# Kernel optimization log

Measured on AMD Instinct MI355X. Metric: run time of the kernel, lower is better.

## Reference

```python
import jax, jax.numpy as jnp
import numpy as np

# Model dims (hardcoded by the hw-accurate numerics: >>6 mean -> d_model=64, 45/256 ~ 1/sqrt(32) -> head_dim=32)
D_MODEL = 64; N_HEADS = 2; HEAD_DIM = 32; D_FF = 256
N_LAYERS = 4; VOCAB = 8192; CTX = 1024; B = 4; T = 1024


def _ste(x, y):
    # forward value y, straight-through gradient of x
    return x + jax.lax.stop_gradient(y - x)


def ste_round_clamp(x, lo, hi):
    return _ste(x, jnp.clip(jnp.round(x), lo, hi))


def ste_round_clamp_int8(x):
    return ste_round_clamp(x, -128.0, 127.0)


def ste_shift_right(x, n):
    s = x * (0.5 ** n)
    return _ste(s, jnp.floor(s))


def ste_hw_int8(x):
    # hardware truncation to signed 8 bits (wrap-around, not clamp)
    return _ste(x, jnp.mod(x + 128.0, 256.0) - 128.0)


def bitlinear_hw(x, w):
    # ternary weights via STE (BitNet b1.58 style), int accumulate, >>6 requant, int8 clamp
    scale = jnp.maximum(jnp.mean(jnp.abs(w)), 1e-5)
    w_t = ste_round_clamp(w / scale, -1.0, 1.0)
    acc = jnp.einsum('btc,oc->bto', x, w_t)
    return ste_round_clamp_int8(ste_shift_right(acc, 6))


def rmsnorm_hw(x, weight):
    x_int = ste_round_clamp_int8(x)
    sum_sq = jnp.sum(x_int * x_int, axis=-1, keepdims=True)
    mean_sq = ste_shift_right(sum_sq, 6)                       # /64 == /d_model
    lut_idx = jnp.clip(ste_shift_right(mean_sq, 6), 0.0, 255.0)
    bin_center = jnp.maximum(lut_idx * 64.0 + 32.0, 1.0)
    inv_rms = ste_round_clamp(16384.0 / jnp.sqrt(bin_center), 0.0, 16383.0)
    w_c = weight + jax.lax.stop_gradient(jnp.clip(weight, -2.0, 2.0) - weight)
    gamma_q = ste_round_clamp(w_c * 1024.0, -32768.0, 32767.0)  # Q5.10
    p1 = ste_shift_right(x_int * inv_rms, 8)
    y = ste_shift_right(p1 * gamma_q, 10)
    return ste_round_clamp_int8(y)


def hw_softmax(scores):
    # 4-segment piecewise-linear exp + uint8 normalization (Softmax.scala)
    m = jnp.max(scores, axis=-1, keepdims=True)
    sh = scores - m
    ea = jnp.where(sh >= -3.0, 256.0 + sh * 64.0,
         jnp.where(sh >= -8.0, 64.0 + (sh + 3.0) * 11.0,
         jnp.where(sh >= -24.0, sh + 24.0, 0.0)))
    s = jnp.maximum(jnp.sum(ea, axis=-1, keepdims=True), 1.0)
    return ste_round_clamp(ea / s * 255.0, 0.0, 255.0)


def _forward(tokens, tok_emb, pos_emb, attn_norm_w, q_w, k_w, v_w, o_w,
             ff_norm_w, up_w, down_w, final_norm_w):
    positions = jnp.arange(T)
    tok_q = ste_round_clamp(tok_emb[tokens] * 1024.0, -32768.0, 32767.0)
    pos_q = ste_round_clamp(pos_emb[positions] * 1024.0, -32768.0, 32767.0)
    x = ste_hw_int8(ste_shift_right(tok_q + pos_q[None], 3))   # [B,T,D]
    causal = jnp.triu(jnp.ones((T, T), dtype=bool), k=1)
    for i in range(N_LAYERS):
        # attention block
        h = rmsnorm_hw(x, attn_norm_w[i])
        q = bitlinear_hw(h, q_w[i]).reshape(B, T, N_HEADS, HEAD_DIM).transpose(0, 2, 1, 3)
        k = bitlinear_hw(h, k_w[i]).reshape(B, T, N_HEADS, HEAD_DIM).transpose(0, 2, 1, 3)
        v = bitlinear_hw(h, v_w[i]).reshape(B, T, N_HEADS, HEAD_DIM).transpose(0, 2, 1, 3)
        scores = ste_shift_right(jnp.einsum('bhqd,bhkd->bhqk', q, k) * 45.0, 8)
        scores = jnp.where(causal, -32767.0, scores)
        probs = hw_softmax(scores)                              # uint8-valued
        a = ste_hw_int8(ste_shift_right(jnp.einsum('bhqk,bhkd->bhqd', probs, v), 8))
        a = a.transpose(0, 2, 1, 3).reshape(B, T, D_MODEL)
        a = bitlinear_hw(a, o_w[i])
        x = ste_hw_int8(x + a)
        # FFN block
        h = rmsnorm_hw(x, ff_norm_w[i])
        u = ste_round_clamp_int8(jax.nn.relu(bitlinear_hw(h, up_w[i])))
        x = ste_hw_int8(x + bitlinear_hw(u, down_w[i]))
    x = rmsnorm_hw(x, final_norm_w)
    # hw logits: INT8 activations x Q5.10 tied embedding, dequant + 1/sqrt(d) scale
    emb_q = ste_round_clamp(tok_emb * 1024.0, -32768.0, 32767.0)
    logits = jnp.einsum('btd,vd->btv', x, emb_q) * (D_MODEL ** -0.5 / 1024.0)
    return logits


def setup_inputs() -> dict:
    key = jax.random.key(0)
    ks = jax.random.split(key, 12)
    std = 0.02
    inp = {
        'tokens': jax.random.randint(ks[0], (B, T), 0, VOCAB),
        'tok_emb': jax.random.normal(ks[1], (VOCAB, D_MODEL), jnp.float32),  # default N(0,1)
        'pos_emb': std * jax.random.normal(ks[2], (CTX, D_MODEL), jnp.float32),
        'attn_norm_w': jnp.ones((N_LAYERS, D_MODEL), jnp.float32),
        'q_w': std * jax.random.normal(ks[3], (N_LAYERS, D_MODEL, D_MODEL), jnp.float32),
        'k_w': std * jax.random.normal(ks[4], (N_LAYERS, D_MODEL, D_MODEL), jnp.float32),
        'v_w': std * jax.random.normal(ks[5], (N_LAYERS, D_MODEL, D_MODEL), jnp.float32),
        'o_w': std * jax.random.normal(ks[6], (N_LAYERS, D_MODEL, D_MODEL), jnp.float32),
        'ff_norm_w': jnp.ones((N_LAYERS, D_MODEL), jnp.float32),
        'up_w': std * jax.random.normal(ks[7], (N_LAYERS, D_FF, D_MODEL), jnp.float32),
        'down_w': std * jax.random.normal(ks[8], (N_LAYERS, D_MODEL, D_FF), jnp.float32),
        'final_norm_w': jnp.ones((D_MODEL,), jnp.float32),
    }
    return inp


def reference(tokens, tok_emb, pos_emb, attn_norm_w, q_w, k_w, v_w, o_w,
              ff_norm_w, up_w, down_w, final_norm_w):
    return _forward(tokens, tok_emb, pos_emb, attn_norm_w, q_w, k_w, v_w, o_w,
                    ff_norm_w, up_w, down_w, final_norm_w)
```

## Files before the change

kernel.cpp:

```cpp
#include <hip/hip_runtime.h>
#include <stdint.h>

#define T_CTX 1024
#define DM 64
#define NH 2
#define HD 32
#define DFF 256
#define NVOCAB 8192

typedef int v4i __attribute__((ext_vector_type(4)));

__device__ __forceinline__ int clampi(int v, int lo, int hi){ return v<lo?lo:(v>hi?hi:v); }
__device__ __forceinline__ int wrap8(int v){ return ((v + 128) & 255) - 128; }
__device__ __forceinline__ int sdot4(int a, int b, int c){ return __builtin_amdgcn_sdot4(a, b, c, false); }

__device__ __forceinline__ int wave_reduce_add(int v){
  #pragma unroll
  for (int off = 1; off < 64; off <<= 1) v += __shfl_xor(v, off, 64);
  return v;
}
__device__ __forceinline__ int wave_reduce_max(int v){
  #pragma unroll
  for (int off = 1; off < 64; off <<= 1){ int o = __shfl_xor(v, off, 64); v = o > v ? o : v; }
  return v;
}

__device__ __forceinline__ int rmsnorm_one(int xv, int g){
  int ss  = wave_reduce_add(xv * xv);
  int ms  = ss >> 6;
  int lut = ms >> 6; if (lut > 255) lut = 255;
  int bc  = lut * 64 + 32;
  int inv = (int)__builtin_rint(16384.0 / __builtin_sqrt((double)bc));
  int p1  = (xv * inv) >> 8;
  int y   = (p1 * g) >> 10;
  return clampi(y, -128, 127);
}

__global__ __launch_bounds__(256) void prep_embed(
    const int* __restrict__ tokens, const float* __restrict__ tok_emb, const float* __restrict__ pos_emb,
    const float* __restrict__ qw, const float* __restrict__ kw, const float* __restrict__ vw,
    const float* __restrict__ ow, const float* __restrict__ uw, const float* __restrict__ dw,
    const float* __restrict__ anw, const float* __restrict__ fnw, const float* __restrict__ finw,
    int8_t* __restrict__ wt, int16_t* __restrict__ gq,
    int8_t* __restrict__ elo, int8_t* __restrict__ ehi,
    int8_t* __restrict__ x, int8_t* __restrict__ qA, int8_t* __restrict__ kA, int8_t* __restrict__ vT)
{
  __shared__ double sred[256];
  __shared__ int8_t sh_h[4][64];
  int tid = threadIdx.x, bid = blockIdx.x;
  if (bid < 24) {
    int layer = bid / 6, kind = bid % 6;
    const float* src; int n; int off;
    switch (kind) {
      case 0:  src = qw + layer*4096;  n = 4096;  off = 0;     break;
      case 1:  src = kw + layer*4096;  n = 4096;  off = 4096;  break;
      case 2:  src = vw + layer*4096;  n = 4096;  off = 8192;  break;
      case 3:  src = ow + layer*4096;  n = 4096;  off = 12288; break;
      case 4:  src = uw + layer*16384; n = 16384; off = 16384; break;
      default: src = dw + layer*16384; n = 16384; off = 32768; break;
    }
    double s = 0.0;
    for (int i = tid; i < n; i += 256) s += (double)__builtin_fabsf(src[i]);
    sred[tid] = s; __syncthreads();
    for (int st = 128; st > 0; st >>= 1){ if (tid < st) sred[tid] += sred[tid + st]; __syncthreads(); }
    float fs = (float)(sred[0] / (double)n);
    if (fs < 1e-5f) fs = 1e-5f;
    int8_t* dst = wt + layer*49152 + off;
    for (int i = tid; i < n; i += 256) {
      int t = (int)__builtin_rintf(src[i] / fs);
      dst[i] = (int8_t)clampi(t, -1, 1);
    }
  } else if (bid == 24) {
    for (int i = tid; i < 576; i += 256) {
      int norm = i >> 6, c = i & 63;
      const float* wsrc = (norm < 4) ? (anw + norm*64) : (norm < 8) ? (fnw + (norm-4)*64) : finw;
      float wv = wsrc[c];
      float wc = wv < -2.0f ? -2.0f : (wv > 2.0f ? 2.0f : wv);
      gq[i] = (int16_t)clampi((int)__builtin_rintf(wc * 1024.0f), -32768, 32767);
    }
  } else if (bid < 2073) {
    int i = (bid - 25)*256 + tid;
    if (i < NVOCAB * DM) {
      int e  = clampi((int)__builtin_rintf(tok_emb[i] * 1024.0f), -32768, 32767);
      int l  = ((e + 128) & 255) - 128;
      int hh = (e - l) >> 8;
      if (hh > 127) hh = 127;
      elo[i] = (int8_t)l; ehi[i] = (int8_t)hh;
    }
  } else {
    int blk = bid - 2073;
    int w = tid >> 6, lane = tid & 63;
    float fss[3];
    const float* srcs[3] = { qw, kw, vw };
    for (int mtx = 0; mtx < 3; mtx++) {
      const float* src = srcs[mtx];
      double s = 0.0;
      for (int i = tid; i < 4096; i += 256) s += (double)__builtin_fabsf(src[i]);
      sred[tid] = s; __syncthreads();
      for (int st = 128; st > 0; st >>= 1){ if (tid < st) sred[tid] += sred[tid + st]; __syncthreads(); }
      float fs = (float)(sred[0] / 4096.0);
      if (fs < 1e-5f) fs = 1e-5f;
      fss[mtx] = fs;
      __syncthreads();
    }
    int wqr[16], wkr[16], wvr[16];
    {
      const float4* rq = (const float4*)(qw + lane*64);
      const float4* rk = (const float4*)(kw + lane*64);
      const float4* rv = (const float4*)(vw + lane*64);
      #pragma unroll
      for (int i = 0; i < 16; i++) {
        float4 f = rq[i];
        int t0 = clampi((int)__builtin_rintf(f.x / fss[0]), -1, 1);
        int t1 = clampi((int)__builtin_rintf(f.y / fss[0]), -1, 1);
        int t2 = clampi((int)__builtin_rintf(f.z / fss[0]), -1, 1);
        int t3 = clampi((int)__builtin_rintf(f.w / fss[0]), -1, 1);
        wqr[i] = (t0&255) | ((t1&255)<<8) | ((t2&255)<<16) | ((t3&255)<<24);
      }
      #pragma unroll
      for (int i = 0; i < 16; i++) {
        float4 f = rk[i];
        int t0 = clampi((int)__builtin_rintf(f.x / fss[1]), -1, 1);
        int t1 = clampi((int)__builtin_rintf(f.y / fss[1]), -1, 1);
        int t2 = clampi((int)__builtin_rintf(f.z / fss[1]), -1, 1);
        int t3 = clampi((int)__builtin_rintf(f.w / fss[1]), -1, 1);
        wkr[i] = (t0&255) | ((t1&255)<<8) | ((t2&255)<<16) | ((t3&255)<<24);
      }
      #pragma unroll
      for (int i = 0; i < 16; i++) {
        float4 f = rv[i];
        int t0 = clampi((int)__builtin_rintf(f.x / fss[2]), -1, 1);
        int t1 = clampi((int)__builtin_rintf(f.y / fss[2]), -1, 1);
        int t2 = clampi((int)__builtin_rintf(f.z / fss[2]), -1, 1);
        int t3 = clampi((int)__builtin_rintf(f.w / fss[2]), -1, 1);
        wvr[i] = (t0&255) | ((t1&255)<<8) | ((t2&255)<<16) | ((t3&255)<<24);
      }
    }
    float gw = anw[lane];
    float gc = gw < -2.0f ? -2.0f : (gw > 2.0f ? 2.0f : gw);
    int g = clampi((int)__builtin_rintf(gc * 1024.0f), -32768, 32767);
    #pragma unroll
    for (int pass = 0; pass < 2; pass++) {
      int t = blk*8 + pass*4 + w;
      int tok = tokens[t];
      int s = t & (T_CTX - 1);
      int tq = clampi((int)__builtin_rintf(tok_emb[tok*DM + lane] * 1024.0f), -32768, 32767);
      int pq = clampi((int)__builtin_rintf(pos_emb[s*DM + lane] * 1024.0f), -32768, 32767);
      int xv = wrap8((tq + pq) >> 3);
      x[t*DM + lane] = (int8_t)xv;
      int h = rmsnorm_one(xv, g);
      sh_h[w][lane] = (int8_t)h;
      const int* h4 = (const int*)sh_h[w];
      int b = t >> 10;
      int hh = lane >> 5, d = lane & 31;
      int bhh = b*NH + hh;
      {
        int acc = 0;
        #pragma unroll
        for (int i = 0; i < 16; i++) acc = sdot4(h4[i], wqr[i], acc);
        qA[(bhh*T_CTX + s)*HD + d] = (int8_t)clampi(acc >> 6, -128, 127);
      }
      {
        int acc = 0;
        #pragma unroll
        for (int i = 0; i < 16; i++) acc = sdot4(h4[i], wkr[i], acc);
        kA[(bhh*T_CTX + s)*HD + d] = (int8_t)clampi(acc >> 6, -128, 127);
      }
      {
        int acc = 0;
        #pragma unroll
        for (int i = 0; i < 16; i++) acc = sdot4(h4[i], wvr[i], acc);
        vT[(bhh*HD + d)*T_CTX + s] = (int8_t)clampi(acc >> 6, -128, 127);
      }
    }
  }
}

__global__ __launch_bounds__(512, 4) void layer_kernel(
    const int8_t* __restrict__ qA, const int8_t* __restrict__ kA, const int8_t* __restrict__ vT,
    int8_t* __restrict__ x, int8_t* __restrict__ qN, int8_t* __restrict__ kN, int8_t* __restrict__ vN,
    const int8_t* __restrict__ wt, const int16_t* __restrict__ gq, int8_t* __restrict__ xf,
    int L, int pre_layer, int do_final)
{
  __shared__ int vt32[64*256];
  __shared__ int sp32[8][256];
  __shared__ int sh_a32[4][16];
  __shared__ int8_t sh8[4][256];

  int tid = threadIdx.x;
  int w = tid >> 6, lane = tid & 63;
  int blk = blockIdx.x;
  int b = blk & 3;
  int s0 = 1020 - 4*(blk >> 2);
  int tl = w >> 1, h = w & 1;
  int qi = s0 + tl;
  int bh = b*NH + h;
  const int8_t* qBase = qA + bh*(T_CTX*HD);
  const int8_t* kBase = kA + bh*(T_CTX*HD);

  #pragma unroll
  for (int r = 0; r < 8; r++) {
    int rr = w*8 + r;
    int slot = rr >> 5, d = rr & 31;
    const int* src = (const int*)(vT + (b*NH + slot)*(HD*T_CTX) + d*T_CTX);
    int xw = ((d >> 2) & 3) << 3;
    int li = lane ^ xw;
    int* dstrow = vt32 + rr*256;
    int v0 = src[lane], v1 = src[lane+64], v2 = src[lane+128], v3 = src[lane+192];
    dstrow[li] = v0; dstrow[li+64] = v1; dstrow[li+128] = v2; dstrow[li+192] = v3;
  }

  const int4* qr = (const int4*)(qBase + qi*HD);
  int4 qa = qr[0], qb = qr[1];
  int sc[16];
  int mloc = -(1 << 30);
  #pragma unroll
  for (int j = 0; j < 16; j++) {
    int k = lane + j*64;
    int s;
    if (k <= qi) {
      const int4* kr = (const int4*)(kBase + k*HD);
      int4 ka = kr[0], kb = kr[1];
      int d = 0;
      d = sdot4(qa.x, ka.x, d); d = sdot4(qa.y, ka.y, d);
      d = sdot4(qa.z, ka.z, d); d = sdot4(qa.w, ka.w, d);
      d = sdot4(qb.x, kb.x, d); d = sdot4(qb.y, kb.y, d);
      d = sdot4(qb.z, kb.z, d); d = sdot4(qb.w, kb.w, d);
      s = (d * 45) >> 8;
    } else s = -(1 << 30);
    sc[j] = s; if (s > mloc) mloc = s;
  }
  int m = wave_reduce_max(mloc);
  int ssum = 0;
  #pragma unroll
  for (int j = 0; j < 16; j++) {
    int k = lane + j*64;
    int e = 0;
    if (k <= qi) {
      int sh = sc[j] - m;
      e = (sh >= -3) ? (256 + sh*64)
        : (sh >= -8) ? (64 + (sh + 3)*11)
        : (sh >= -24) ? (sh + 24) : 0;
    }
    sc[j] = e; ssum += e;
  }
  int s0sum = wave_reduce_add(ssum); if (s0sum < 1) s0sum = 1;
  float sf = (float)s0sum;
  uint8_t* spb = (uint8_t*)sp32[w];
  #pragma unroll
  for (int j = 0; j < 16; j++) {
    int k = lane + j*64;
    int p = (int)__builtin_rintf((float)sc[j] / sf * 255.0f);
    spb[k] = (uint8_t)clampi(p, 0, 255);
  }
  __syncthreads();

  int dg = lane & 7, kc = lane >> 3;
  int xw = (dg & 3) << 3;
  const int* vr0 = vt32 + (h*32 + dg*4 + 0)*256;
  const int* vr1 = vt32 + (h*32 + dg*4 + 1)*256;
  const int* vr2 = vt32 + (h*32 + dg*4 + 2)*256;
  const int* vr3 = vt32 + (h*32 + dg*4 + 3)*256;
  const int* spw = sp32[w];
  int hi0=0, hi1=0, hi2=0, hi3=0, lo0=0, lo1=0, lo2=0, lo3=0;
  int cmax = qi >> 2;
  for (int c = kc; c <= cmax; c += 8) {
    int p4 = spw[c];
    int cs = c ^ xw;
    int ph = (p4 >> 1) & 0x7f7f7f7f;
    int pl = p4 & 0x01010101;
    int v0 = vr0[cs], v1 = vr1[cs], v2 = vr2[cs], v3 = vr3[cs];
    hi0 = sdot4(ph, v0, hi0); lo0 = sdot4(pl, v0, lo0);
    hi1 = sdot4(ph, v1, hi1); lo1 = sdot4(pl, v1, lo1);
    hi2 = sdot4(ph, v2, hi2); lo2 = sdot4(pl, v2, lo2);
    hi3 = sdot4(ph, v3, hi3); lo3 = sdot4(pl, v3, lo3);
  }
  int a0 = 2*hi0 + lo0, a1 = 2*hi1 + lo1, a2 = 2*hi2 + lo2, a3 = 2*hi3 + lo3;
  #pragma unroll
  for (int off = 8; off < 64; off <<= 1) {
    a0 += __shfl_xor(a0, off, 64);
    a1 += __shfl_xor(a1, off, 64);
    a2 += __shfl_xor(a2, off, 64);
    a3 += __shfl_xor(a3, off, 64);
  }
  if (kc == 0) {
    int r0 = wrap8(a0 >> 8) & 255;
    int r1 = wrap8(a1 >> 8) & 255;
    int r2 = wrap8(a2 >> 8) & 255;
    int r3 = wrap8(a3 >> 8) & 255;
    int packed = r0 | (r1 << 8) | (r2 << 16) | (r3 << 24);
    sh_a32[tl][h*8 + dg] = packed;
  }
  __syncthreads();

  if (w < 4) {
    int t = b*T_CTX + s0 + w;
    const int8_t* wtL = wt + L*49152;
    int xv = (int)x[t*DM + lane];
    {
      const int* a4 = sh_a32[w];
      const int* wo = (const int*)(wtL + 12288);
      int acc = 0;
      #pragma unroll
      for (int i = 0; i < 16; i++) acc = sdot4(a4[i], wo[lane*16 + i], acc);
      xv = wrap8(xv + clampi(acc >> 6, -128, 127));
    }
    int h2 = rmsnorm_one(xv, (int)gq[(4 + L)*DM + lane]);
    int8_t* myS = sh8[w];
    myS[lane] = (int8_t)h2;
    const int* h4 = (const int*)myS;
    int uv[4];
    {
      const int* wu = (const int*)(wtL + 16384);
      #pragma unroll
      for (int jj = 0; jj < 4; jj++) {
        int j = jj*64 + lane;
        int acc = 0;
        #pragma unroll
        for (int i = 0; i < 16; i++) acc = sdot4(h4[i], wu[j*16 + i], acc);
        int u = clampi(acc >> 6, -128, 127);
        uv[jj] = u < 0 ? 0 : u;
      }
    }
    #pragma unroll
    for (int jj = 0; jj < 4; jj++) myS[jj*64 + lane] = (int8_t)uv[jj];
    {
      const int* u4 = (const int*)myS;
      const int* wd = (const int*)(wtL + 32768);
      int acc = 0;
      #pragma unroll
      for (int i = 0; i < 64; i++) acc = sdot4(u4[i], wd[lane*64 + i], acc);
      xv = wrap8(xv + clampi(acc >> 6, -128, 127));
    }
    x[t*DM + lane] = (int8_t)xv;
    if (pre_layer >= 0) {
      int hp = rmsnorm_one(xv, (int)gq[pre_layer*DM + lane]);
      myS[lane] = (int8_t)hp;
      const int* hp4 = (const int*)myS;
      const int8_t* wtP = wt + pre_layer*49152;
      int s = s0 + w;
      int hh = lane >> 5, d = lane & 31;
      int bhh = b*NH + hh;
      {
        const int* wm = (const int*)(wtP + 0);
        int acc = 0;
        #pragma unroll
        for (int i = 0; i < 16; i++) acc = sdot4(hp4[i], wm[lane*16 + i], acc);
        qN[(bhh*T_CTX + s)*HD + d] = (int8_t)clampi(acc >> 6, -128, 127);
      }
      {
        const int* wm = (const int*)(wtP + 4096);
        int acc = 0;
        #pragma unroll
        for (int i = 0; i < 16; i++) acc = sdot4(hp4[i], wm[lane*16 + i], acc);
        kN[(bhh*T_CTX + s)*HD + d] = (int8_t)clampi(acc >> 6, -128, 127);
      }
      {
        const int* wm = (const int*)(wtP + 8192);
        int acc = 0;
        #pragma unroll
        for (int i = 0; i < 16; i++) acc = sdot4(hp4[i], wm[lane*16 + i], acc);
        vN[(bhh*HD + d)*T_CTX + s] = (int8_t)clampi(acc >> 6, -128, 127);
      }
    }
    if (do_final) {
      int hf = rmsnorm_one(xv, (int)gq[8*DM + lane]);
      xf[t*DM + lane] = (int8_t)hf;
    }
  }
}

__global__ __launch_bounds__(256) void logits_kernel(
    const int8_t* __restrict__ xf, const int8_t* __restrict__ elo, const int8_t* __restrict__ ehi,
    float* __restrict__ out)
{
  int w = threadIdx.x >> 6, lane = threadIdx.x & 63;
  int m = lane & 15, quad = lane >> 4;
  int tokBase = blockIdx.y * 64 + w * 16;
  v4i Bx = *(const v4i*)(xf + (tokBase + m)*DM + quad*16);
  float* orow = out + (tokBase + m)*NVOCAB;
  #pragma unroll
  for (int tile = 0; tile < 8; tile++) {
    int vocBase = blockIdx.x * 128 + tile * 16;
    v4i Alo = *(const v4i*)(elo + (vocBase + m)*DM + quad*16);
    v4i Ahi = *(const v4i*)(ehi + (vocBase + m)*DM + quad*16);
    v4i zero = {0, 0, 0, 0};
    v4i dLo = __builtin_amdgcn_mfma_i32_16x16x64_i8(Alo, Bx, zero, 0, 0, 0);
    v4i dHi = __builtin_amdgcn_mfma_i32_16x16x64_i8(Ahi, Bx, zero, 0, 0, 0);
    float4 o;
    o.x = (float)(dLo[0] + (dHi[0] << 8)) * 1.220703125e-4f;
    o.y = (float)(dLo[1] + (dHi[1] << 8)) * 1.220703125e-4f;
    o.z = (float)(dLo[2] + (dHi[2] << 8)) * 1.220703125e-4f;
    o.w = (float)(dLo[3] + (dHi[3] << 8)) * 1.220703125e-4f;
    *(float4*)(orow + vocBase + quad*4) = o;
  }
}

extern "C" void kernel_launch(void* const* d_in, const int* in_sizes, int n_in,
                              void* d_out, int out_size, void* d_ws, size_t ws_size,
                              hipStream_t stream)
{
  const int*   tokens  = (const int*)d_in[0];
  const float* tok_emb = (const float*)d_in[1];
  const float* pos_emb = (const float*)d_in[2];
  const float* attn_nw = (const float*)d_in[3];
  const float* q_w     = (const float*)d_in[4];
  const float* k_w     = (const float*)d_in[5];
  const float* v_w     = (const float*)d_in[6];
  const float* o_w     = (const float*)d_in[7];
  const float* ff_nw   = (const float*)d_in[8];
  const float* up_w    = (const float*)d_in[9];
  const float* dn_w    = (const float*)d_in[10];
  const float* fin_nw  = (const float*)d_in[11];
  float* out = (float*)d_out;
  char* ws = (char*)d_ws;

  int8_t*  x    = (int8_t*)(ws + 0);
  int8_t*  qA0  = (int8_t*)(ws + 262144);
  int8_t*  kA0  = (int8_t*)(ws + 524288);
  int8_t*  vT0  = (int8_t*)(ws + 786432);
  int8_t*  qA1  = (int8_t*)(ws + 1048576);
  int8_t*  kA1  = (int8_t*)(ws + 1310720);
  int8_t*  vT1  = (int8_t*)(ws + 1572864);
  int8_t*  wt   = (int8_t*)(ws + 1835008);
  int8_t*  elo  = (int8_t*)(ws + 2031616);
  int8_t*  ehi  = (int8_t*)(ws + 2555904);
  int16_t* gq   = (int16_t*)(ws + 3080192);
  int8_t*  xf   = (int8_t*)(ws + 3081344);

  prep_embed<<<2585, 256, 0, stream>>>(tokens, tok_emb, pos_emb,
                                       q_w, k_w, v_w, o_w, up_w, dn_w, attn_nw, ff_nw, fin_nw,
                                       wt, gq, elo, ehi, x, qA0, kA0, vT0);
  for (int L = 0; L < 4; L++) {
    int8_t* qC = (L & 1) ? qA1 : qA0;  int8_t* qX = (L & 1) ? qA0 : qA1;
    int8_t* kC = (L & 1) ? kA1 : kA0;  int8_t* kX = (L & 1) ? kA0 : kA1;
    int8_t* vC = (L & 1) ? vT1 : vT0;  int8_t* vX = (L & 1) ? vT0 : vT1;
    int pre = (L < 3) ? (L + 1) : -1;
    int fin = (L == 3) ? 1 : 0;
    layer_kernel<<<1024, 512, 0, stream>>>(qC, kC, vC, x, qX, kX, vX, wt, gq, xf, L, pre, fin);
  }
  logits_kernel<<<dim3(64, 64), 256, 0, stream>>>(xf, elo, ehi, out);
}
```

Measured before the change: 343.5 us.

## Process eight query rows per layer block, looping heads per wave

Each layer block now handles 8 query positions instead of 4, with each wave computing both heads for its token in turn rather than one head per wave. The 64-row V tile staged into shared memory is therefore reused across twice as many queries and the grid is halved, and all 8 waves now run the post-attention MLP instead of only 4. The embedding-split prep is also vectorised to float4 loads and packed 4-byte stores, cutting its block count. The trade-off is less parallelism per block (serial heads per wave) and half as many blocks for the GPU to spread across its compute units.

```diff
diff --git a/kernel.cpp b/kernel.cpp
--- a/kernel.cpp
+++ b/kernel.cpp
@@ -78,17 +78,21 @@
       float wc = wv < -2.0f ? -2.0f : (wv > 2.0f ? 2.0f : wv);
       gq[i] = (int16_t)clampi((int)__builtin_rintf(wc * 1024.0f), -32768, 32767);
     }
-  } else if (bid < 2073) {
-    int i = (bid - 25)*256 + tid;
-    if (i < NVOCAB * DM) {
-      int e  = clampi((int)__builtin_rintf(tok_emb[i] * 1024.0f), -32768, 32767);
-      int l  = ((e + 128) & 255) - 128;
-      int hh = (e - l) >> 8;
-      if (hh > 127) hh = 127;
-      elo[i] = (int8_t)l; ehi[i] = (int8_t)hh;
-    }
+  } else if (bid < 537) {
+    int i4 = (bid - 25)*1024 + tid*4;
+    float4 f = *(const float4*)(tok_emb + i4);
+    int e0 = clampi((int)__builtin_rintf(f.x * 1024.0f), -32768, 32767);
+    int e1 = clampi((int)__builtin_rintf(f.y * 1024.0f), -32768, 32767);
+    int e2 = clampi((int)__builtin_rintf(f.z * 1024.0f), -32768, 32767);
+    int e3 = clampi((int)__builtin_rintf(f.w * 1024.0f), -32768, 32767);
+    int l0 = ((e0 + 128) & 255) - 128, l1 = ((e1 + 128) & 255) - 128;
+    int l2 = ((e2 + 128) & 255) - 128, l3 = ((e3 + 128) & 255) - 128;
+    int h0 = (e0 - l0) >> 8, h1 = (e1 - l1) >> 8;
+    int h2 = (e2 - l2) >> 8, h3 = (e3 - l3) >> 8;
+    *(int*)(elo + i4) = (l0&255) | ((l1&255)<<8) | ((l2&255)<<16) | ((l3&255)<<24);
+    *(int*)(ehi + i4) = (h0&255) | ((h1&255)<<8) | ((h2&255)<<16) | ((h3&255)<<24);
   } else {
-    int blk = bid - 2073;
+    int blk = bid - 537;
     int w = tid >> 6, lane = tid & 63;
     float fss[3];
     const float* srcs[3] = { qw, kw, vw };
@@ -184,19 +188,15 @@
 {
   __shared__ int vt32[64*256];
   __shared__ int sp32[8][256];
-  __shared__ int sh_a32[4][16];
-  __shared__ int8_t sh8[4][256];
+  __shared__ int sh_a32[8][16];
+  __shared__ int8_t sh8[8][256];
 
   int tid = threadIdx.x;
   int w = tid >> 6, lane = tid & 63;
   int blk = blockIdx.x;
   int b = blk & 3;
-  int s0 = 1020 - 4*(blk >> 2);
-  int tl = w >> 1, h = w & 1;
-  int qi = s0 + tl;
-  int bh = b*NH + h;
-  const int8_t* qBase = qA + bh*(T_CTX*HD);
-  const int8_t* kBase = kA + bh*(T_CTX*HD);
+  int s0 = 1016 - 8*(blk >> 2);
+  int qi = s0 + w;
 
   #pragma unroll
   for (int r = 0; r < 8; r++) {
@@ -210,90 +210,96 @@
     dstrow[li] = v0; dstrow[li+64] = v1; dstrow[li+128] = v2; dstrow[li+192] = v3;
   }
 
-  const int4* qr = (const int4*)(qBase + qi*HD);
-  int4 qa = qr[0], qb = qr[1];
-  int sc[16];
-  int mloc = -(1 << 30);
-  #pragma unroll
-  for (int j = 0; j < 16; j++) {
-    int k = lane + j*64;
-    int s;
-    if (k <= qi) {
-      const int4* kr = (const int4*)(kBase + k*HD);
-      int4 ka = kr[0], kb = kr[1];
-      int d = 0;
-      d = sdot4(qa.x, ka.x, d); d = sdot4(qa.y, ka.y, d);
-      d = sdot4(qa.z, ka.z, d); d = sdot4(qa.w, ka.w, d);
-      d = sdot4(qb.x, kb.x, d); d = sdot4(qb.y, kb.y, d);
-      d = sdot4(qb.z, kb.z, d); d = sdot4(qb.w, kb.w, d);
-      s = (d * 45) >> 8;
-    } else s = -(1 << 30);
-    sc[j] = s; if (s > mloc) mloc = s;
-  }
-  int m = wave_reduce_max(mloc);
-  int ssum = 0;
-  #pragma unroll
-  for (int j = 0; j < 16; j++) {
-    int k = lane + j*64;
-    int e = 0;
-    if (k <= qi) {
-      int sh = sc[j] - m;
-      e = (sh >= -3) ? (256 + sh*64)
-        : (sh >= -8) ? (64 + (sh + 3)*11)
-        : (sh >= -24) ? (sh + 24) : 0;
-    }
-    sc[j] = e; ssum += e;
-  }
-  int s0sum = wave_reduce_add(ssum); if (s0sum < 1) s0sum = 1;
-  float sf = (float)s0sum;
+  int dg = lane & 7, kc = lane >> 3;
+  int xw2 = (dg & 3) << 3;
+  const int* spw = sp32[w];
   uint8_t* spb = (uint8_t*)sp32[w];
-  #pragma unroll
-  for (int j = 0; j < 16; j++) {
-    int k = lane + j*64;
-    int p = (int)__builtin_rintf((float)sc[j] / sf * 255.0f);
-    spb[k] = (uint8_t)clampi(p, 0, 255);
-  }
-  __syncthreads();
-
-  int dg = lane & 7, kc = lane >> 3;
-  int xw = (dg & 3) << 3;
-  const int* vr0 = vt32 + (h*32 + dg*4 + 0)*256;
-  const int* vr1 = vt32 + (h*32 + dg*4 + 1)*256;
-  const int* vr2 = vt32 + (h*32 + dg*4 + 2)*256;
-  const int* vr3 = vt32 + (h*32 + dg*4 + 3)*256;
-  const int* spw = sp32[w];
-  int hi0=0, hi1=0, hi2=0, hi3=0, lo0=0, lo1=0, lo2=0, lo3=0;
-  int cmax = qi >> 2;
-  for (int c = kc; c <= cmax; c += 8) {
-    int p4 = spw[c];
-    int cs = c ^ xw;
-    int ph = (p4 >> 1) & 0x7f7f7f7f;
-    int pl = p4 & 0x01010101;
-    int v0 = vr0[cs], v1 = vr1[cs], v2 = vr2[cs], v3 = vr3[cs];
-    hi0 = sdot4(ph, v0, hi0); lo0 = sdot4(pl, v0, lo0);
-    hi1 = sdot4(ph, v1, hi1); lo1 = sdot4(pl, v1, lo1);
-    hi2 = sdot4(ph, v2, hi2); lo2 = sdot4(pl, v2, lo2);
-    hi3 = sdot4(ph, v3, hi3); lo3 = sdot4(pl, v3, lo3);
-  }
-  int a0 = 2*hi0 + lo0, a1 = 2*hi1 + lo1, a2 = 2*hi2 + lo2, a3 = 2*hi3 + lo3;
-  #pragma unroll
-  for (int off = 8; off < 64; off <<= 1) {
-    a0 += __shfl_xor(a0, off, 64);
-    a1 += __shfl_xor(a1, off, 64);
-    a2 += __shfl_xor(a2, off, 64);
-    a3 += __shfl_xor(a3, off, 64);
-  }
-  if (kc == 0) {
-    int r0 = wrap8(a0 >> 8) & 255;
-    int r1 = wrap8(a1 >> 8) & 255;
-    int r2 = wrap8(a2 >> 8) & 255;
-    int r3 = wrap8(a3 >> 8) & 255;
-    int packed = r0 | (r1 << 8) | (r2 << 16) | (r3 << 24);
-    sh_a32[tl][h*8 + dg] = packed;
-  }
-  __syncthreads();
-
-  if (w < 4) {
+
+  for (int h = 0; h < 2; h++) {
+    int bh = b*NH + h;
+    const int8_t* qBase = qA + bh*(T_CTX*HD);
+    const int8_t* kBase = kA + bh*(T_CTX*HD);
+
+    const int4* qr = (const int4*)(qBase + qi*HD);
+    int4 qa = qr[0], qb = qr[1];
+    int sc[16];
+    int mloc = -(1 << 30);
+    #pragma unroll
+    for (int j = 0; j < 16; j++) {
+      int k = lane + j*64;
+      int s;
+      if (k <= qi) {
+        const int4* kr = (const int4*)(kBase + k*HD);
+        int4 ka = kr[0], kb = kr[1];
+        int d = 0;
+        d = sdot4(qa.x, ka.x, d); d = sdot4(qa.y, ka.y, d);
+        d = sdot4(qa.z, ka.z, d); d = sdot4(qa.w, ka.w, d);
+        d = sdot4(qb.x, kb.x, d); d = sdot4(qb.y, kb.y, d);
+        d = sdot4(qb.z, kb.z, d); d = sdot4(qb.w, kb.w, d);
+        s = (d * 45) >> 8;
+      } else s = -(1 << 30);
+      sc[j] = s; if (s > mloc) mloc = s;
+    }
+    int m = wave_reduce_max(mloc);
+    int ssum = 0;
+    #pragma unroll
+    for (int j = 0; j < 16; j++) {
+      int k = lane + j*64;
+      int e = 0;
+      if (k <= qi) {
+        int sh = sc[j] - m;
+        e = (sh >= -3) ? (256 + sh*64)
+          : (sh >= -8) ? (64 + (sh + 3)*11)
+          : (sh >= -24) ? (sh + 24) : 0;
+      }
+      sc[j] = e; ssum += e;
+    }
+    int s0sum = wave_reduce_add(ssum); if (s0sum < 1) s0sum = 1;
+    float sf = (float)s0sum;
+    #pragma unroll
+    for (int j = 0; j < 16; j++) {
+      int k = lane + j*64;
+      int p = (int)__builtin_rintf((float)sc[j] / sf * 255.0f);
+      spb[k] = (uint8_t)clampi(p, 0, 255);
+    }
+    if (h == 0) __syncthreads();
+
+    const int* vr0 = vt32 + (h*32 + dg*4 + 0)*256;
+    const int* vr1 = vt32 + (h*32 + dg*4 + 1)*256;
+    const int* vr2 = vt32 + (h*32 + dg*4 + 2)*256;
+    const int* vr3 = vt32 + (h*32 + dg*4 + 3)*256;
+    int hi0=0, hi1=0, hi2=0, hi3=0, lo0=0, lo1=0, lo2=0, lo3=0;
+    int cmax = qi >> 2;
+    for (int c = kc; c <= cmax; c += 8) {
+      int p4 = spw[c];
+      int cs = c ^ xw2;
+      int ph = (p4 >> 1) & 0x7f7f7f7f;
+      int pl = p4 & 0x01010101;
+      int v0 = vr0[cs], v1 = vr1[cs], v2 = vr2[cs], v3 = vr3[cs];
+      hi0 = sdot4(ph, v0, hi0); lo0 = sdot4(pl, v0, lo0);
+      hi1 = sdot4(ph, v1, hi1); lo1 = sdot4(pl, v1, lo1);
+      hi2 = sdot4(ph, v2, hi2); lo2 = sdot4(pl, v2, lo2);
+      hi3 = sdot4(ph, v3, hi3); lo3 = sdot4(pl, v3, lo3);
+    }
+    int a0 = 2*hi0 + lo0, a1 = 2*hi1 + lo1, a2 = 2*hi2 + lo2, a3 = 2*hi3 + lo3;
+    #pragma unroll
+    for (int off = 8; off < 64; off <<= 1) {
+      a0 += __shfl_xor(a0, off, 64);
+      a1 += __shfl_xor(a1, off, 64);
+      a2 += __shfl_xor(a2, off, 64);
+      a3 += __shfl_xor(a3, off, 64);
+    }
+    if (kc == 0) {
+      int r0 = wrap8(a0 >> 8) & 255;
+      int r1 = wrap8(a1 >> 8) & 255;
+      int r2 = wrap8(a2 >> 8) & 255;
+      int r3 = wrap8(a3 >> 8) & 255;
+      int packed = r0 | (r1 << 8) | (r2 << 16) | (r3 << 24);
+      sh_a32[w][h*8 + dg] = packed;
+    }
+  }
+
+  {
     int t = b*T_CTX + s0 + w;
     const int8_t* wtL = wt + L*49152;
     int xv = (int)x[t*DM + lane];
@@ -428,7 +434,7 @@
   int16_t* gq   = (int16_t*)(ws + 3080192);
   int8_t*  xf   = (int8_t*)(ws + 3081344);
 
-  prep_embed<<<2585, 256, 0, stream>>>(tokens, tok_emb, pos_emb,
+  prep_embed<<<1049, 256, 0, stream>>>(tokens, tok_emb, pos_emb,
                                        q_w, k_w, v_w, o_w, up_w, dn_w, attn_nw, ff_nw, fin_nw,
                                        wt, gq, elo, ehi, x, qA0, kA0, vT0);
   for (int L = 0; L < 4; L++) {
@@ -437,7 +443,7 @@
     int8_t* vC = (L & 1) ? vT1 : vT0;  int8_t* vX = (L & 1) ? vT0 : vT1;
     int pre = (L < 3) ? (L + 1) : -1;
     int fin = (L == 3) ? 1 : 0;
-    layer_kernel<<<1024, 512, 0, stream>>>(qC, kC, vC, x, qX, kX, vX, wt, gq, xf, L, pre, fin);
+    layer_kernel<<<512, 512, 0, stream>>>(qC, kC, vC, x, qX, kX, vX, wt, gq, xf, L, pre, fin);
   }
   logits_kernel<<<dim3(64, 64), 256, 0, stream>>>(xf, elo, ehi, out);
 }
```

Result: faster. 325.1 us (-5.4%).
